# Performance work log

Measured on AMD Instinct MI355X. Metric: run time of the kernel, lower is better.

Reference implementation:

```python
import jax, jax.numpy as jnp
import numpy as np

DELTA = 5.0          # weight on positive BCE term
R = 0.01             # hard-negative fraction
M, N = 4096, 16384   # batch rows, memory-bank size
NUM_HARD = int(R * (N - 1))  # int(r * neg_count); each row has exactly 1 positive


def setup_inputs() -> dict:
    key = jax.random.key(0)
    k1, k2 = jax.random.split(key)
    inputs = jax.random.normal(k1, (M, N), dtype=jnp.float32)
    targets = jax.random.randint(k2, (M,), 0, N)
    return {"inputs": inputs, "targets": targets}


def reference(inputs, targets):
    m, n = inputs.shape
    rows = jnp.arange(m)
    # positive logit per row (one-hot scatter => exactly one positive)
    pos = inputs[rows, targets]                          # [m]
    # BCE with logits, target=1: softplus(-x); mean over the single positive
    l_pos = jax.nn.softplus(-pos)                        # [m]
    # exclude positive from negatives by sinking it to -inf, then hard top-k
    neg_inf = jnp.finfo(inputs.dtype).min
    masked = inputs.at[rows, targets].set(neg_inf)       # [m, n]
    hard_neg, _ = jax.lax.top_k(masked, NUM_HARD)        # [m, NUM_HARD]
    # BCE with logits, target=0: softplus(x); mean over hard negatives
    l_neg = jnp.mean(jax.nn.softplus(hard_neg), axis=1)  # [m]
    return jnp.mean(DELTA * l_pos + l_neg)
```

## Files before the change

kernel.cpp:

```cpp
#include <hip/hip_runtime.h>
#include <stdint.h>

#define M_ROWS 4096
#define N_COLS 16384
#define K_HARD 163
#define DELTA_W 5.0f
#define CAP    5376
#define NB1    4096
#define NB2    1024
#define BLOCK  256

__device__ __forceinline__ uint32_t f2key(float x) {
    uint32_t u = __float_as_uint(x);
    return (u & 0x80000000u) ? ~u : (u | 0x80000000u);
}
__device__ __forceinline__ float key2f(uint32_t k) {
    uint32_t u = (k & 0x80000000u) ? (k & 0x7fffffffu) : ~k;
    return __uint_as_float(u);
}
__device__ __forceinline__ float softplus_f(float x) {
    return fmaxf(x, 0.0f) + log1pf(__expf(-fabsf(x)));
}

__device__ void pivot_scan(const uint32_t* hist, int nb, int K,
                           int* part, int* pivot, int* krem) {
    const int t = threadIdx.x;
    const int bpt = nb / BLOCK;
    const int base = t * bpt;
    int mypart = 0;
    for (int i = 0; i < bpt; ++i) mypart += (int)hist[base + i];
    part[t] = mypart;
    __syncthreads();
    for (int off = 1; off < BLOCK; off <<= 1) {
        int v = part[t];
        if (t + off < BLOCK) v += part[t + off];
        __syncthreads();
        part[t] = v;
        __syncthreads();
    }
    const int above = part[t] - mypart;
    if (above < K && above + mypart >= K) {
        int running = above;
        for (int b = base + bpt - 1; b >= base; --b) {
            int c = (int)hist[b];
            if (running < K && running + c >= K) { *pivot = b; *krem = K - running; }
            running += c;
        }
    }
    __syncthreads();
}

__global__ __launch_bounds__(BLOCK) void mmcl_kernel(
        const float* __restrict__ inputs,
        const int* __restrict__ targets,
        float* __restrict__ out) {
    __shared__ uint32_t s_hist[NB1];
    __shared__ uint32_t s_cand[CAP];
    __shared__ int s_part[BLOCK];
    __shared__ int s_ncand;
    __shared__ int s_pivot;
    __shared__ int s_krem;
    __shared__ float s_pos;
    __shared__ float s_wsum[BLOCK / 64];

    const int row = blockIdx.x;
    const int t = threadIdx.x;
    const int lane = t & 63;
    const float* rowp = inputs + (size_t)row * N_COLS;
    const int target = targets[row];

    for (int i = t; i < NB1; i += BLOCK) s_hist[i] = 0;
    if (t == 0) s_ncand = 0;
    __syncthreads();

    const uint32_t KEY_MIN = 0xBF800000u;

    const float4* rp4 = (const float4*)rowp;
    for (int it = 0; it < N_COLS / (BLOCK * 4); ++it) {
        const int v4 = it * BLOCK + t;
        const float4 v = rp4[v4];
        const int j0 = v4 * 4;
        const float vals[4] = {v.x, v.y, v.z, v.w};
#pragma unroll
        for (int c = 0; c < 4; ++c) {
            const int j = j0 + c;
            const float x = vals[c];
            const bool is_t = (j == target);
            if (is_t) s_pos = x;
            const uint32_t key = f2key(x);
            const bool pred = (!is_t) && (key >= KEY_MIN);
            const unsigned long long mask = __ballot(pred);
            if (mask) {
                const int leader = __ffsll((unsigned long long)mask) - 1;
                const int cnt = __popcll(mask);
                int basei = 0;
                if (lane == leader) basei = atomicAdd(&s_ncand, cnt);
                basei = __shfl(basei, leader);
                if (pred) {
                    const int off = basei +
                        (int)__popcll(mask & ((1ULL << lane) - 1ULL));
                    if (off < CAP) s_cand[off] = key;
                }
            }
        }
    }
    __syncthreads();
    const int ncand = s_ncand;
    const bool fast = (ncand >= K_HARD) && (ncand <= CAP);

    float local = 0.0f;
    uint32_t T;
    int tie;

    if (fast) {
        for (int i = t; i < ncand; i += BLOCK)
            atomicAdd(&s_hist[s_cand[i] >> 20], 1u);
        __syncthreads();
        pivot_scan(s_hist, NB1, K_HARD, s_part, &s_pivot, &s_krem);
        const int p1 = s_pivot, k1 = s_krem;

        for (int i = t; i < NB2; i += BLOCK) s_hist[i] = 0;
        __syncthreads();
        for (int i = t; i < ncand; i += BLOCK) {
            const uint32_t k = s_cand[i];
            if ((int)(k >> 20) == p1) atomicAdd(&s_hist[(k >> 10) & 1023u], 1u);
        }
        __syncthreads();
        pivot_scan(s_hist, NB2, k1, s_part, &s_pivot, &s_krem);
        const int p2 = s_pivot, k2 = s_krem;
        const uint32_t pref2 = ((uint32_t)p1 << 10) | (uint32_t)p2;

        for (int i = t; i < NB2; i += BLOCK) s_hist[i] = 0;
        __syncthreads();
        for (int i = t; i < ncand; i += BLOCK) {
            const uint32_t k = s_cand[i];
            if ((k >> 10) == pref2) atomicAdd(&s_hist[k & 1023u], 1u);
        }
        __syncthreads();
        pivot_scan(s_hist, NB2, k2, s_part, &s_pivot, &s_krem);
        T = (pref2 << 10) | (uint32_t)s_pivot;
        tie = s_krem;

        for (int i = t; i < ncand; i += BLOCK) {
            const uint32_t k = s_cand[i];
            if (k > T) local += softplus_f(key2f(k));
        }
    } else {
        for (int j = t; j < N_COLS; j += BLOCK) {
            if (j == target) continue;
            atomicAdd(&s_hist[f2key(rowp[j]) >> 20], 1u);
        }
        __syncthreads();
        pivot_scan(s_hist, NB1, K_HARD, s_part, &s_pivot, &s_krem);
        const int p1 = s_pivot, k1 = s_krem;

        for (int i = t; i < NB2; i += BLOCK) s_hist[i] = 0;
        __syncthreads();
        for (int j = t; j < N_COLS; j += BLOCK) {
            if (j == target) continue;
            const uint32_t k = f2key(rowp[j]);
            if ((int)(k >> 20) == p1) atomicAdd(&s_hist[(k >> 10) & 1023u], 1u);
        }
        __syncthreads();
        pivot_scan(s_hist, NB2, k1, s_part, &s_pivot, &s_krem);
        const int p2 = s_pivot, k2 = s_krem;
        const uint32_t pref2 = ((uint32_t)p1 << 10) | (uint32_t)p2;

        for (int i = t; i < NB2; i += BLOCK) s_hist[i] = 0;
        __syncthreads();
        for (int j = t; j < N_COLS; j += BLOCK) {
            if (j == target) continue;
            const uint32_t k = f2key(rowp[j]);
            if ((k >> 10) == pref2) atomicAdd(&s_hist[k & 1023u], 1u);
        }
        __syncthreads();
        pivot_scan(s_hist, NB2, k2, s_part, &s_pivot, &s_krem);
        T = (pref2 << 10) | (uint32_t)s_pivot;
        tie = s_krem;

        for (int j = t; j < N_COLS; j += BLOCK) {
            if (j == target) continue;
            const uint32_t k = f2key(rowp[j]);
            if (k > T) local += softplus_f(key2f(k));
        }
    }

    for (int off = 32; off > 0; off >>= 1) local += __shfl_down(local, off);
    if (lane == 0) s_wsum[t >> 6] = local;
    __syncthreads();
    if (t == 0) {
        float tot = 0.0f;
        for (int w = 0; w < BLOCK / 64; ++w) tot += s_wsum[w];
        tot += (float)tie * softplus_f(key2f(T));
        const float l_neg = tot / (float)K_HARD;
        const float l_pos = softplus_f(-s_pos);
        const float rowval = (DELTA_W * l_pos + l_neg) * (1.0f / (float)M_ROWS);
        atomicAdd(out, rowval);
    }
}

__global__ void mmcl_zero_out(float* out) { out[0] = 0.0f; }

extern "C" void kernel_launch(void* const* d_in, const int* in_sizes, int n_in,
                              void* d_out, int out_size, void* d_ws, size_t ws_size,
                              hipStream_t stream) {
    const float* inputs = (const float*)d_in[0];
    const int* targets = (const int*)d_in[1];
    float* out = (float*)d_out;
    mmcl_zero_out<<<1, 1, 0, stream>>>(out);
    mmcl_kernel<<<M_ROWS, BLOCK, 0, stream>>>(inputs, targets, out);
}
```

Baseline: 429.3 us.

## Tighten candidate threshold, drop per-element ballot, remove positive after filtering

```diff
diff --git a/kernel.cpp b/kernel.cpp
--- a/kernel.cpp
+++ b/kernel.cpp
@@ -5,14 +5,14 @@
 #define N_COLS 16384
 #define K_HARD 163
 #define DELTA_W 5.0f
-#define CAP    5376
+#define CAP    1024
 #define NB1    4096
 #define NB2    1024
 #define BLOCK  256
 
 __device__ __forceinline__ uint32_t f2key(float x) {
     uint32_t u = __float_as_uint(x);
-    return (u & 0x80000000u) ? ~u : (u | 0x80000000u);
+    return u ^ (((int32_t)u >> 31) | 0x80000000u);
 }
 __device__ __forceinline__ float key2f(uint32_t k) {
     uint32_t u = (k & 0x80000000u) ? (k & 0x7fffffffu) : ~k;
@@ -21,6 +21,8 @@
 __device__ __forceinline__ float softplus_f(float x) {
     return fmaxf(x, 0.0f) + log1pf(__expf(-fabsf(x)));
 }
+
+#define KEY_MIN 0xC0000000u
 
 __device__ void pivot_scan(const uint32_t* hist, int nb, int K,
                            int* part, int* pivot, int* krem) {
@@ -58,6 +60,7 @@
     __shared__ uint32_t s_cand[CAP];
     __shared__ int s_part[BLOCK];
     __shared__ int s_ncand;
+    __shared__ int s_found;
     __shared__ int s_pivot;
     __shared__ int s_krem;
     __shared__ float s_pos;
@@ -70,43 +73,37 @@
     const int target = targets[row];
 
     for (int i = t; i < NB1; i += BLOCK) s_hist[i] = 0;
-    if (t == 0) s_ncand = 0;
-    __syncthreads();
-
-    const uint32_t KEY_MIN = 0xBF800000u;
+    if (t == 0) { s_ncand = 0; s_found = -1; s_pos = rowp[target]; }
+    __syncthreads();
 
     const float4* rp4 = (const float4*)rowp;
+#pragma unroll 4
     for (int it = 0; it < N_COLS / (BLOCK * 4); ++it) {
-        const int v4 = it * BLOCK + t;
-        const float4 v = rp4[v4];
-        const int j0 = v4 * 4;
-        const float vals[4] = {v.x, v.y, v.z, v.w};
-#pragma unroll
-        for (int c = 0; c < 4; ++c) {
-            const int j = j0 + c;
-            const float x = vals[c];
-            const bool is_t = (j == target);
-            if (is_t) s_pos = x;
-            const uint32_t key = f2key(x);
-            const bool pred = (!is_t) && (key >= KEY_MIN);
-            const unsigned long long mask = __ballot(pred);
-            if (mask) {
-                const int leader = __ffsll((unsigned long long)mask) - 1;
-                const int cnt = __popcll(mask);
-                int basei = 0;
-                if (lane == leader) basei = atomicAdd(&s_ncand, cnt);
-                basei = __shfl(basei, leader);
-                if (pred) {
-                    const int off = basei +
-                        (int)__popcll(mask & ((1ULL << lane) - 1ULL));
-                    if (off < CAP) s_cand[off] = key;
-                }
-            }
-        }
+        const float4 v = rp4[it * BLOCK + t];
+        const uint32_t k0 = f2key(v.x), k1 = f2key(v.y),
+                       k2 = f2key(v.z), k3 = f2key(v.w);
+        if (k0 >= KEY_MIN) { int i = atomicAdd(&s_ncand, 1); if (i < CAP) s_cand[i] = k0; }
+        if (k1 >= KEY_MIN) { int i = atomicAdd(&s_ncand, 1); if (i < CAP) s_cand[i] = k1; }
+        if (k2 >= KEY_MIN) { int i = atomicAdd(&s_ncand, 1); if (i < CAP) s_cand[i] = k2; }
+        if (k3 >= KEY_MIN) { int i = atomicAdd(&s_ncand, 1); if (i < CAP) s_cand[i] = k3; }
+    }
+    __syncthreads();
+
+    const int ncand_raw = s_ncand;
+    const uint32_t tkey = f2key(s_pos);
+    const bool no_ovf = (ncand_raw <= CAP);
+    if (no_ovf && tkey >= KEY_MIN) {
+        for (int i = t; i < ncand_raw; i += BLOCK)
+            if (s_cand[i] == tkey) { atomicCAS(&s_found, -1, i); break; }
+    }
+    __syncthreads();
+    if (t == 0 && s_found >= 0) {
+        s_cand[s_found] = s_cand[ncand_raw - 1];
+        s_ncand = ncand_raw - 1;
     }
     __syncthreads();
     const int ncand = s_ncand;
-    const bool fast = (ncand >= K_HARD) && (ncand <= CAP);
+    const bool fast = no_ovf && (ncand >= K_HARD);
 
     float local = 0.0f;
     uint32_t T;
@@ -117,7 +114,7 @@
             atomicAdd(&s_hist[s_cand[i] >> 20], 1u);
         __syncthreads();
         pivot_scan(s_hist, NB1, K_HARD, s_part, &s_pivot, &s_krem);
-        const int p1 = s_pivot, k1 = s_krem;
+        const int p1 = s_pivot, k1r = s_krem;
 
         for (int i = t; i < NB2; i += BLOCK) s_hist[i] = 0;
         __syncthreads();
@@ -126,8 +123,8 @@
             if ((int)(k >> 20) == p1) atomicAdd(&s_hist[(k >> 10) & 1023u], 1u);
         }
         __syncthreads();
-        pivot_scan(s_hist, NB2, k1, s_part, &s_pivot, &s_krem);
-        const int p2 = s_pivot, k2 = s_krem;
+        pivot_scan(s_hist, NB2, k1r, s_part, &s_pivot, &s_krem);
+        const int p2 = s_pivot, k2r = s_krem;
         const uint32_t pref2 = ((uint32_t)p1 << 10) | (uint32_t)p2;
 
         for (int i = t; i < NB2; i += BLOCK) s_hist[i] = 0;
@@ -137,7 +134,7 @@
             if ((k >> 10) == pref2) atomicAdd(&s_hist[k & 1023u], 1u);
         }
         __syncthreads();
-        pivot_scan(s_hist, NB2, k2, s_part, &s_pivot, &s_krem);
+        pivot_scan(s_hist, NB2, k2r, s_part, &s_pivot, &s_krem);
         T = (pref2 << 10) | (uint32_t)s_pivot;
         tie = s_krem;
 
@@ -146,13 +143,15 @@
             if (k > T) local += softplus_f(key2f(k));
         }
     } else {
+        for (int i = t; i < NB1; i += BLOCK) s_hist[i] = 0;
+        __syncthreads();
         for (int j = t; j < N_COLS; j += BLOCK) {
             if (j == target) continue;
             atomicAdd(&s_hist[f2key(rowp[j]) >> 20], 1u);
         }
         __syncthreads();
         pivot_scan(s_hist, NB1, K_HARD, s_part, &s_pivot, &s_krem);
-        const int p1 = s_pivot, k1 = s_krem;
+        const int p1 = s_pivot, k1r = s_krem;
 
         for (int i = t; i < NB2; i += BLOCK) s_hist[i] = 0;
         __syncthreads();
@@ -162,8 +161,8 @@
             if ((int)(k >> 20) == p1) atomicAdd(&s_hist[(k >> 10) & 1023u], 1u);
         }
         __syncthreads();
-        pivot_scan(s_hist, NB2, k1, s_part, &s_pivot, &s_krem);
-        const int p2 = s_pivot, k2 = s_krem;
+        pivot_scan(s_hist, NB2, k1r, s_part, &s_pivot, &s_krem);
+        const int p2 = s_pivot, k2r = s_krem;
         const uint32_t pref2 = ((uint32_t)p1 << 10) | (uint32_t)p2;
 
         for (int i = t; i < NB2; i += BLOCK) s_hist[i] = 0;
@@ -174,7 +173,7 @@
             if ((k >> 10) == pref2) atomicAdd(&s_hist[k & 1023u], 1u);
         }
         __syncthreads();
-        pivot_scan(s_hist, NB2, k2, s_part, &s_pivot, &s_krem);
+        pivot_scan(s_hist, NB2, k2r, s_part, &s_pivot, &s_krem);
         T = (pref2 << 10) | (uint32_t)s_pivot;
         tie = s_krem;
 
```

After: 400.3 us. 6.8% less time.
